# Kernel optimization log

Hardware: AMD Instinct MI355X
Metric: run time of the kernel (lower is better)

Reference implementation:

```python
import jax, jax.numpy as jnp
import numpy as np

N = 50000
E = 800000
C = 128   # embed_channels
H = 4     # num_heads
D = C // H
POS = 3


def setup_inputs() -> dict:
    key = jax.random.key(0)
    ks = jax.random.split(key, 8)
    feat = jax.random.normal(ks[0], (N, C), dtype=jnp.float32)
    coord = jax.random.normal(ks[1], (N, POS), dtype=jnp.float32)
    graph = jax.random.randint(ks[2], (2, E), 0, N, dtype=jnp.int32)
    qkv_w = jax.random.normal(ks[3], (3 * C, C), dtype=jnp.float32) * (1.0 / np.sqrt(C))
    qkv_b = jax.random.normal(ks[4], (3 * C,), dtype=jnp.float32) * 0.02
    rpe_w = jax.random.normal(ks[5], (C, POS), dtype=jnp.float32) * (1.0 / np.sqrt(POS))
    rpe_b = jax.random.normal(ks[6], (C,), dtype=jnp.float32) * 0.02
    return {"feat": feat, "coord": coord, "graph": graph,
            "qkv_w": qkv_w, "qkv_b": qkv_b, "rpe_w": rpe_w, "rpe_b": rpe_b}


def _segment_softmax(x, seg, n):
    # x: [E, H], seg: [E] -> softmax over edges sharing the same destination node
    seg_max = jax.ops.segment_max(x, seg, num_segments=n)          # [N, H]
    seg_max = jnp.where(jnp.isfinite(seg_max), seg_max, 0.0)
    ex = jnp.exp(x - seg_max[seg])                                 # [E, H]
    seg_sum = jax.ops.segment_sum(ex, seg, num_segments=n)         # [N, H]
    return ex / seg_sum[seg]


def reference(feat, coord, graph, qkv_w, qkv_b, rpe_w, rpe_b):
    n = feat.shape[0]
    # qkv projection: [N, 3C] -> [N, 3, H, D]
    qkv = (feat @ qkv_w.T + qkv_b).reshape(n, 3, H, D)
    query, key, value = qkv[:, 0], qkv[:, 1], qkv[:, 2]            # each [N, H, D]
    dst, src = graph[0], graph[1]                                  # [E]
    # relative position encoding per edge
    rel = coord[dst] - coord[src]                                  # [E, 3]
    rpe = (rel @ rpe_w.T + rpe_b).reshape(-1, H, D)                # [E, H, D]
    # per-edge attention logits
    attn = (key[src] * query[dst] + rpe).sum(-1)                   # [E, H]
    attn = _segment_softmax(attn, dst, n)                          # [E, H]
    # weighted scatter-sum of values
    msg = attn[..., None] * value[src]                             # [E, H, D]
    out = jax.ops.segment_sum(msg, dst, num_segments=n)            # [N, H, D]
    return out.reshape(n, H * D)
```

## Files before the change

kernel.cpp:

```cpp
#include <hip/hip_runtime.h>
#include <hip/hip_bf16.h>

#define NN 50000
#define NE 800000
#define PAD 64
#define CAB 196
#define NBK 391
#define CAPB 2560
#define GB_STRIDE 32

typedef _Float16 fp16x8 __attribute__((ext_vector_type(8)));
typedef _Float16 half2 __attribute__((ext_vector_type(2)));
typedef __attribute__((ext_vector_type(8))) unsigned short ushort8;
typedef __attribute__((ext_vector_type(4))) float f32x4;

static __device__ __forceinline__ unsigned short f2h(float x) {
    _Float16 h = (_Float16)x;
    return __builtin_bit_cast(unsigned short, h);
}
static __device__ __forceinline__ float dot2(half2 a, half2 b, float c) {
#if __has_builtin(__builtin_amdgcn_fdot2)
    return __builtin_amdgcn_fdot2(a, b, c, false);
#else
    return c + (float)a.x * (float)b.x + (float)a.y * (float)b.y;
#endif
}

__global__ __launch_bounds__(256) void qkv_gemm(
    const float* __restrict__ feat, const float* __restrict__ w,
    const float* __restrict__ bias, unsigned short* __restrict__ qbuf16,
    unsigned short* __restrict__ kvbuf,
    const float* __restrict__ coord, const float* __restrict__ rpe_w,
    const float* __restrict__ rpe_b, float* __restrict__ ca,
    float* __restrict__ cb,
    const int* __restrict__ graph, unsigned int* __restrict__ gbase,
    unsigned int* __restrict__ ebuf)
{
    const int t    = threadIdx.x;
    const int role = blockIdx.x & 3;
    const int bi   = blockIdx.x >> 2;

    __shared__ __align__(16) unsigned short Ah[128][40];
    __shared__ __align__(16) unsigned short Bh[128][40];

    if (role == 3) {
        unsigned int* hist  = (unsigned int*)&Ah[0][0];
        unsigned int* sbase = hist + 512;
        for (int u = t; u < NBK; u += 256) hist[u] = 0u;
        __syncthreads();

        int dsts[8], srcs[8];
        bool ok[8];
        const int e0 = bi * 2048;
#pragma unroll
        for (int u = 0; u < 8; ++u) {
            int e = e0 + u * 256 + t;
            ok[u] = (e < NE);
            if (ok[u]) { dsts[u] = graph[e]; srcs[u] = graph[NE + e]; }
        }
#pragma unroll
        for (int u = 0; u < 8; ++u)
            if (ok[u]) atomicAdd(&hist[dsts[u] >> 7], 1u);
        __syncthreads();
        for (int u = t; u < NBK; u += 256) {
            unsigned int c = hist[u];
            unsigned int s = c ? atomicAdd(&gbase[u * GB_STRIDE], c) : 0u;
            sbase[u] = s;
            hist[u]  = 0u;
        }
        __syncthreads();
#pragma unroll
        for (int u = 0; u < 8; ++u)
            if (ok[u]) {
                int b = dsts[u] >> 7;
                unsigned int pos = sbase[b] + atomicAdd(&hist[b], 1u);
                if (pos < CAPB)
                    ebuf[(size_t)b * CAPB + pos] =
                        ((unsigned int)(dsts[u] & 127) << 16) | (unsigned int)srcs[u];
            }

        if (bi < CAB) {
            __shared__ float s_rw[12];
            __shared__ float s_rb[4];
            if (t < 12) {
                int h = t / 3, p = t % 3;
                float s = 0.f;
                for (int d = 0; d < 32; ++d) s += rpe_w[(h * 32 + d) * 3 + p];
                s_rw[t] = s;
            } else if (t < 16) {
                int h = t - 12;
                float s = 0.f;
                for (int d = 0; d < 32; ++d) s += rpe_b[h * 32 + d];
                s_rb[h] = s;
            }
            __syncthreads();
            int n = bi * 256 + t;
            if (n < NN) {
                float c0 = coord[n * 3 + 0], c1 = coord[n * 3 + 1], c2 = coord[n * 3 + 2];
#pragma unroll
                for (int h = 0; h < 4; ++h) {
                    float a = c0 * s_rw[h * 3 + 0] + c1 * s_rw[h * 3 + 1] + c2 * s_rw[h * 3 + 2];
                    ca[n * 4 + h] = a;
                    cb[n * 4 + h] = a + s_rb[h];
                }
            }
        }
        return;
    }

    const int bm = bi * 128;
    const int bc = role * 128;

    const int wave = t >> 6;
    const int lane = t & 63;
    const int wr = wave & 1;
    const int wc = wave >> 1;
    const int qd = lane >> 4;
    const int l15 = lane & 15;

    f32x4 acc[4][4];
#pragma unroll
    for (int i = 0; i < 4; ++i)
#pragma unroll
        for (int j = 0; j < 4; ++j)
            acc[i][j] = (f32x4){0.f, 0.f, 0.f, 0.f};

    for (int ks = 0; ks < 4; ++ks) {
        const int k0 = ks * 32;
        if (ks) __syncthreads();
#pragma unroll
        for (int c = 0; c < 2; ++c) {
            int idx = c * 256 + t;
            int r  = idx >> 2;
            int c8 = (idx & 3) * 8;
            int ga = bm + r;
            ushort8 a8 = (ushort8){0,0,0,0,0,0,0,0};
            if (ga < NN) {
                const float* ap = feat + (size_t)ga * 128 + k0 + c8;
                float4 x = *(const float4*)ap;
                float4 y = *(const float4*)(ap + 4);
                a8 = (ushort8){f2h(x.x), f2h(x.y), f2h(x.z), f2h(x.w),
                               f2h(y.x), f2h(y.y), f2h(y.z), f2h(y.w)};
            }
            *(ushort8*)&Ah[r][c8] = a8;
            const float* bp = w + (size_t)(bc + r) * 128 + k0 + c8;
            float4 bx = *(const float4*)bp;
            float4 by = *(const float4*)(bp + 4);
            *(ushort8*)&Bh[r][c8] = (ushort8){f2h(bx.x), f2h(bx.y), f2h(bx.z), f2h(bx.w),
                                              f2h(by.x), f2h(by.y), f2h(by.z), f2h(by.w)};
        }
        __syncthreads();
        fp16x8 af[4];
#pragma unroll
        for (int i = 0; i < 4; ++i)
            af[i] = *(const fp16x8*)&Ah[wr * 64 + 16 * i + l15][qd * 8];
#pragma unroll
        for (int j = 0; j < 4; ++j) {
            fp16x8 bf = *(const fp16x8*)&Bh[wc * 64 + 16 * j + l15][qd * 8];
#pragma unroll
            for (int i = 0; i < 4; ++i)
                acc[i][j] = __builtin_amdgcn_mfma_f32_16x16x32_f16(af[i], bf, acc[i][j], 0, 0, 0);
        }
    }

    float bj[4];
#pragma unroll
    for (int j = 0; j < 4; ++j)
        bj[j] = bias[bc + wc * 64 + 16 * j + l15];

    unsigned short* Ct = &Ah[0][0];
    const int isQ = (role == 0);
    const int half = (role == 1) ? 0 : 128;
    const int relRowW = wr * 16 + qd * 4;

    for (int i = 0; i < 4; ++i) {
        __syncthreads();
#pragma unroll
        for (int j = 0; j < 4; ++j) {
            int col = wc * 64 + 16 * j + l15;
#pragma unroll
            for (int rg = 0; rg < 4; ++rg)
                Ct[(relRowW + rg) * 136 + col] = f2h(acc[i][j][rg] + bj[j]);
        }
        __syncthreads();
#pragma unroll
        for (int p = 0; p < 2; ++p) {
            int linear = p * 256 + t;
            int rr = linear >> 4;
            int cc = linear & 15;
            int absRow = bm + 16 * i + rr + ((rr >> 4) * 48);
            if (absRow < NN) {
                ushort8 val = *(const ushort8*)&Ct[rr * 136 + cc * 8];
                if (isQ) *(ushort8*)(qbuf16 + (size_t)absRow * 128 + cc * 8) = val;
                else     *(ushort8*)(kvbuf + (size_t)absRow * 256 + half + cc * 8) = val;
            }
        }
    }
}

__global__ __launch_bounds__(256) void bucket_to_csr(
    const unsigned int* __restrict__ gbase, const unsigned int* __restrict__ ebuf,
    int* __restrict__ cnt, unsigned short* __restrict__ sorted_src)
{
    __shared__ unsigned int ncnt[128];
    const int b = blockIdx.x;
    const int t = threadIdx.x;
    if (t < 128) ncnt[t] = 0u;
    __syncthreads();

    int total = (int)gbase[b * GB_STRIDE];
    if (total > CAPB) total = CAPB;
    const unsigned int* eb = ebuf + (size_t)b * CAPB;
    for (int i = t; i < total; i += 256) {
        unsigned int e = eb[i];
        int dl = (int)(e >> 16);
        unsigned int slot = atomicAdd(&ncnt[dl], 1u);
        if (slot < PAD)
            sorted_src[(((size_t)(b * 128 + dl)) << 6) + slot] =
                (unsigned short)(e & 0xFFFFu);
    }
    __syncthreads();
    if (t < 128) {
        int node = b * 128 + t;
        if (node < NN) {
            unsigned int c = ncnt[t];
            cnt[node] = (c > PAD) ? PAD : (int)c;
        }
    }
}

__global__ __launch_bounds__(256) void node_attn(
    const unsigned short* __restrict__ qbuf16, const unsigned short* __restrict__ kvbuf,
    const float* __restrict__ ca, const float* __restrict__ cb,
    const int* __restrict__ cnt, const unsigned short* __restrict__ sorted_src,
    float* __restrict__ out)
{
    const int t = threadIdx.x;
    const int n = blockIdx.x * 8 + (t >> 5);
    if (n >= NN) return;
    const int j = t & 31;
    const int h = j >> 3;
    const int j8 = j * 8;
    const int h4 = h * 4;

    const uint2 qv = *(const uint2*)((const char*)qbuf16 + (size_t)n * 256 + j8);
    const half2 qh01 = __builtin_bit_cast(half2, qv.x);
    const half2 qh23 = __builtin_bit_cast(half2, qv.y);
    const float cbh = cb[n * 4 + h];
    const int start = n << 6;
    int d = cnt[n];
    if (d > PAD) d = PAD;

    float4 acc = make_float4(0.f, 0.f, 0.f, 0.f);
    float den = 0.f;
    const char* kvp = (const char*)kvbuf;
    const char* cap = (const char*)ca;

    int i = 0;
    for (; i + 7 < d; i += 8) {
        ushort8 s8 = *(const ushort8*)(sorted_src + start + i);
        unsigned o[8];
#pragma unroll
        for (int u = 0; u < 8; ++u) o[u] = (unsigned)s8[u] << 9;
        uint2 kk[8], vv[8];
        float aa[8];
#pragma unroll
        for (int u = 0; u < 8; ++u) kk[u] = *(const uint2*)(kvp + o[u] + j8);
#pragma unroll
        for (int u = 0; u < 8; ++u) vv[u] = *(const uint2*)(kvp + o[u] + 256 + j8);
#pragma unroll
        for (int u = 0; u < 8; ++u) aa[u] = *(const float*)(cap + (o[u] >> 5) + h4);
        float p[8];
#pragma unroll
        for (int u = 0; u < 8; ++u)
            p[u] = dot2(qh01, __builtin_bit_cast(half2, kk[u].x),
                   dot2(qh23, __builtin_bit_cast(half2, kk[u].y), 0.f));
#pragma unroll
        for (int u = 0; u < 8; ++u) p[u] += __shfl_xor(p[u], 1);
#pragma unroll
        for (int u = 0; u < 8; ++u) p[u] += __shfl_xor(p[u], 2);
#pragma unroll
        for (int u = 0; u < 8; ++u) p[u] += __shfl_xor(p[u], 4);
        float e[8];
#pragma unroll
        for (int u = 0; u < 8; ++u) { e[u] = __expf(p[u] + cbh - aa[u]); den += e[u]; }
#pragma unroll
        for (int u = 0; u < 8; ++u) {
            half2 va = __builtin_bit_cast(half2, vv[u].x);
            half2 vb = __builtin_bit_cast(half2, vv[u].y);
            acc.x += e[u] * (float)va.x;
            acc.y += e[u] * (float)va.y;
            acc.z += e[u] * (float)vb.x;
            acc.w += e[u] * (float)vb.y;
        }
    }
    for (; i + 3 < d; i += 4) {
        ushort4 s4 = *(const ushort4*)(sorted_src + start + i);
        unsigned o0 = (unsigned)s4.x << 9;
        unsigned o1 = (unsigned)s4.y << 9;
        unsigned o2 = (unsigned)s4.z << 9;
        unsigned o3 = (unsigned)s4.w << 9;
        uint2 k0 = *(const uint2*)(kvp + o0 + j8);
        uint2 k1 = *(const uint2*)(kvp + o1 + j8);
        uint2 k2 = *(const uint2*)(kvp + o2 + j8);
        uint2 k3 = *(const uint2*)(kvp + o3 + j8);
        uint2 v0 = *(const uint2*)(kvp + o0 + 256 + j8);
        uint2 v1 = *(const uint2*)(kvp + o1 + 256 + j8);
        uint2 v2 = *(const uint2*)(kvp + o2 + 256 + j8);
        uint2 v3 = *(const uint2*)(kvp + o3 + 256 + j8);
        float a0 = *(const float*)(cap + (o0 >> 5) + h4);
        float a1 = *(const float*)(cap + (o1 >> 5) + h4);
        float a2 = *(const float*)(cap + (o2 >> 5) + h4);
        float a3 = *(const float*)(cap + (o3 >> 5) + h4);

        float p0 = dot2(qh01, __builtin_bit_cast(half2, k0.x),
                   dot2(qh23, __builtin_bit_cast(half2, k0.y), 0.f));
        float p1 = dot2(qh01, __builtin_bit_cast(half2, k1.x),
                   dot2(qh23, __builtin_bit_cast(half2, k1.y), 0.f));
        float p2 = dot2(qh01, __builtin_bit_cast(half2, k2.x),
                   dot2(qh23, __builtin_bit_cast(half2, k2.y), 0.f));
        float p3 = dot2(qh01, __builtin_bit_cast(half2, k3.x),
                   dot2(qh23, __builtin_bit_cast(half2, k3.y), 0.f));
        p0 += __shfl_xor(p0, 1); p1 += __shfl_xor(p1, 1);
        p2 += __shfl_xor(p2, 1); p3 += __shfl_xor(p3, 1);
        p0 += __shfl_xor(p0, 2); p1 += __shfl_xor(p1, 2);
        p2 += __shfl_xor(p2, 2); p3 += __shfl_xor(p3, 2);
        p0 += __shfl_xor(p0, 4); p1 += __shfl_xor(p1, 4);
        p2 += __shfl_xor(p2, 4); p3 += __shfl_xor(p3, 4);

        float e0 = __expf(p0 + cbh - a0);
        float e1 = __expf(p1 + cbh - a1);
        float e2 = __expf(p2 + cbh - a2);
        float e3 = __expf(p3 + cbh - a3);
        den += (e0 + e1) + (e2 + e3);
        half2 v0a = __builtin_bit_cast(half2, v0.x), v0b = __builtin_bit_cast(half2, v0.y);
        half2 v1a = __builtin_bit_cast(half2, v1.x), v1b = __builtin_bit_cast(half2, v1.y);
        half2 v2a = __builtin_bit_cast(half2, v2.x), v2b = __builtin_bit_cast(half2, v2.y);
        half2 v3a = __builtin_bit_cast(half2, v3.x), v3b = __builtin_bit_cast(half2, v3.y);
        acc.x += e0 * (float)v0a.x + e1 * (float)v1a.x + e2 * (float)v2a.x + e3 * (float)v3a.x;
        acc.y += e0 * (float)v0a.y + e1 * (float)v1a.y + e2 * (float)v2a.y + e3 * (float)v3a.y;
        acc.z += e0 * (float)v0b.x + e1 * (float)v1b.x + e2 * (float)v2b.x + e3 * (float)v3b.x;
        acc.w += e0 * (float)v0b.y + e1 * (float)v1b.y + e2 * (float)v2b.y + e3 * (float)v3b.y;
    }
    for (; i < d; ++i) {
        unsigned o0 = (unsigned)sorted_src[start + i] << 9;
        uint2 k0 = *(const uint2*)(kvp + o0 + j8);
        uint2 v0 = *(const uint2*)(kvp + o0 + 256 + j8);
        float a0 = *(const float*)(cap + (o0 >> 5) + h4);
        float p0 = dot2(qh01, __builtin_bit_cast(half2, k0.x),
                   dot2(qh23, __builtin_bit_cast(half2, k0.y), 0.f));
        p0 += __shfl_xor(p0, 1);
        p0 += __shfl_xor(p0, 2);
        p0 += __shfl_xor(p0, 4);
        float e = __expf(p0 + cbh - a0);
        den += e;
        half2 va = __builtin_bit_cast(half2, v0.x);
        half2 vb = __builtin_bit_cast(half2, v0.y);
        acc.x += e * (float)va.x;
        acc.y += e * (float)va.y;
        acc.z += e * (float)vb.x;
        acc.w += e * (float)vb.y;
    }

    float inv = (den > 0.f) ? 1.0f / den : 0.f;
    float4 o = make_float4(acc.x * inv, acc.y * inv, acc.z * inv, acc.w * inv);
    ((float4*)(out + (size_t)n * 128))[j] = o;
}

extern "C" void kernel_launch(void* const* d_in, const int* in_sizes, int n_in,
                              void* d_out, int out_size, void* d_ws, size_t ws_size,
                              hipStream_t stream) {
    const float* feat  = (const float*)d_in[0];
    const float* coord = (const float*)d_in[1];
    const int*   graph = (const int*)d_in[2];
    const float* qkv_w = (const float*)d_in[3];
    const float* qkv_b = (const float*)d_in[4];
    const float* rpe_w = (const float*)d_in[5];
    const float* rpe_b = (const float*)d_in[6];
    float* out = (float*)d_out;

    unsigned short* qbuf16 = (unsigned short*)d_ws;
    unsigned short* kvbuf  = qbuf16 + (size_t)NN * 128;
    int*            cnt    = (int*)(kvbuf + (size_t)NN * 256);
    unsigned short* sorted_src = (unsigned short*)(cnt + NN);
    float* ca = (float*)(sorted_src + (size_t)NN * PAD);
    float* cb = ca + (size_t)NN * 4;
    unsigned int* gbase = (unsigned int*)(cb + (size_t)NN * 4);
    unsigned int* ebuf  = gbase + (size_t)NBK * GB_STRIDE;

    hipMemsetAsync(gbase, 0, (size_t)NBK * GB_STRIDE * sizeof(unsigned int), stream);

    qkv_gemm <<<dim3(391 * 4), 256, 0, stream>>>(feat, qkv_w, qkv_b, qbuf16, kvbuf,
                                                 coord, rpe_w, rpe_b, ca, cb,
                                                 graph, gbase, ebuf);
    bucket_to_csr<<<dim3(NBK), 256, 0, stream>>>(gbase, ebuf, cnt, sorted_src);
    node_attn<<<dim3((NN + 7) / 8), 256, 0, stream>>>(qbuf16, kvbuf, ca, cb,
                                                      cnt, sorted_src, out);
}
```

Measured before the change: 185.7 us.

## Split attention into score and output kernels with head-major K/V layout

K and V are now stored head-major, as separate [H][N][32] fp16 arrays instead of one interleaved [N][256] buffer. The fused node attention kernel is split into two. The first computes per-edge exp scores per head and stores them with the inverse denominators in a workspace buffer. The second gathers V per head and accumulates the output. The head-major layout gives each pass a smaller gather footprint that fits better in cache, at the cost of an extra launch, a round trip of the score buffer through memory, and a second read of the CSR indices.

Result: slower. 225.5 us (+21.4%).

```diff
diff --git a/kernel.cpp b/kernel.cpp
--- a/kernel.cpp
+++ b/kernel.cpp
@@ -8,6 +8,8 @@
 #define NBK 391
 #define CAPB 2560
 #define GB_STRIDE 32
+#define NCHUNK 1563
+#define NPAIR 782
 
 typedef _Float16 fp16x8 __attribute__((ext_vector_type(8)));
 typedef _Float16 half2 __attribute__((ext_vector_type(2)));
@@ -25,11 +27,14 @@
     return c + (float)a.x * (float)b.x + (float)a.y * (float)b.y;
 #endif
 }
+static __device__ __forceinline__ half2 h2(unsigned u) {
+    return __builtin_bit_cast(half2, u);
+}
 
 __global__ __launch_bounds__(256) void qkv_gemm(
     const float* __restrict__ feat, const float* __restrict__ w,
     const float* __restrict__ bias, unsigned short* __restrict__ qbuf16,
-    unsigned short* __restrict__ kvbuf,
+    unsigned short* __restrict__ kh, unsigned short* __restrict__ vh,
     const float* __restrict__ coord, const float* __restrict__ rpe_w,
     const float* __restrict__ rpe_b, float* __restrict__ ca,
     float* __restrict__ cb,
@@ -170,7 +175,7 @@
 
     unsigned short* Ct = &Ah[0][0];
     const int isQ = (role == 0);
-    const int half = (role == 1) ? 0 : 128;
+    unsigned short* kv_dst = (role == 1) ? kh : vh;
     const int relRowW = wr * 16 + qd * 4;
 
     for (int i = 0; i < 4; ++i) {
@@ -191,8 +196,12 @@
             int absRow = bm + 16 * i + rr + ((rr >> 4) * 48);
             if (absRow < NN) {
                 ushort8 val = *(const ushort8*)&Ct[rr * 136 + cc * 8];
-                if (isQ) *(ushort8*)(qbuf16 + (size_t)absRow * 128 + cc * 8) = val;
-                else     *(ushort8*)(kvbuf + (size_t)absRow * 256 + half + cc * 8) = val;
+                if (isQ) {
+                    *(ushort8*)(qbuf16 + (size_t)absRow * 128 + cc * 8) = val;
+                } else {
+                    size_t off = (size_t)(cc >> 2) * NN * 32 + (size_t)absRow * 32 + (cc & 3) * 8;
+                    *(ushort8*)(kv_dst + off) = val;
+                }
             }
         }
     }
@@ -229,142 +238,127 @@
     }
 }
 
-__global__ __launch_bounds__(256) void node_attn(
-    const unsigned short* __restrict__ qbuf16, const unsigned short* __restrict__ kvbuf,
+__global__ __launch_bounds__(256) void attn_score(
+    const unsigned short* __restrict__ qbuf16, const unsigned short* __restrict__ kh,
     const float* __restrict__ ca, const float* __restrict__ cb,
     const int* __restrict__ cnt, const unsigned short* __restrict__ sorted_src,
-    float* __restrict__ out)
+    float* __restrict__ ebufE, float* __restrict__ invden)
 {
     const int t = threadIdx.x;
-    const int n = blockIdx.x * 8 + (t >> 5);
+    const int x = blockIdx.x & 7;
+    const int h = x >> 1;
+    const int chunk = (blockIdx.x >> 3) * 2 + (x & 1);
+    const int n = chunk * 32 + (t >> 3);
     if (n >= NN) return;
-    const int j = t & 31;
-    const int h = j >> 3;
-    const int j8 = j * 8;
-    const int h4 = h * 4;
-
-    const uint2 qv = *(const uint2*)((const char*)qbuf16 + (size_t)n * 256 + j8);
-    const half2 qh01 = __builtin_bit_cast(half2, qv.x);
-    const half2 qh23 = __builtin_bit_cast(half2, qv.y);
+    const int l  = t & 7;
+    const int l4 = l * 4;
+
+    const uint2 qv = *(const uint2*)(qbuf16 + (size_t)n * 128 + h * 32 + l4);
+    const half2 q01 = h2(qv.x), q23 = h2(qv.y);
     const float cbh = cb[n * 4 + h];
-    const int start = n << 6;
+    const unsigned short* sl  = sorted_src + ((size_t)n << 6);
+    const unsigned short* khp = kh + (size_t)h * NN * 32;
+    float* erow = ebufE + ((size_t)h * NN + n) * 64;
     int d = cnt[n];
-    if (d > PAD) d = PAD;
-
-    float4 acc = make_float4(0.f, 0.f, 0.f, 0.f);
+
     float den = 0.f;
-    const char* kvp = (const char*)kvbuf;
-    const char* cap = (const char*)ca;
-
     int i = 0;
-    for (; i + 7 < d; i += 8) {
-        ushort8 s8 = *(const ushort8*)(sorted_src + start + i);
-        unsigned o[8];
-#pragma unroll
-        for (int u = 0; u < 8; ++u) o[u] = (unsigned)s8[u] << 9;
-        uint2 kk[8], vv[8];
-        float aa[8];
-#pragma unroll
-        for (int u = 0; u < 8; ++u) kk[u] = *(const uint2*)(kvp + o[u] + j8);
-#pragma unroll
-        for (int u = 0; u < 8; ++u) vv[u] = *(const uint2*)(kvp + o[u] + 256 + j8);
-#pragma unroll
-        for (int u = 0; u < 8; ++u) aa[u] = *(const float*)(cap + (o[u] >> 5) + h4);
-        float p[8];
-#pragma unroll
-        for (int u = 0; u < 8; ++u)
-            p[u] = dot2(qh01, __builtin_bit_cast(half2, kk[u].x),
-                   dot2(qh23, __builtin_bit_cast(half2, kk[u].y), 0.f));
-#pragma unroll
-        for (int u = 0; u < 8; ++u) p[u] += __shfl_xor(p[u], 1);
-#pragma unroll
-        for (int u = 0; u < 8; ++u) p[u] += __shfl_xor(p[u], 2);
-#pragma unroll
-        for (int u = 0; u < 8; ++u) p[u] += __shfl_xor(p[u], 4);
-        float e[8];
-#pragma unroll
-        for (int u = 0; u < 8; ++u) { e[u] = __expf(p[u] + cbh - aa[u]); den += e[u]; }
-#pragma unroll
-        for (int u = 0; u < 8; ++u) {
-            half2 va = __builtin_bit_cast(half2, vv[u].x);
-            half2 vb = __builtin_bit_cast(half2, vv[u].y);
-            acc.x += e[u] * (float)va.x;
-            acc.y += e[u] * (float)va.y;
-            acc.z += e[u] * (float)vb.x;
-            acc.w += e[u] * (float)vb.y;
-        }
-    }
     for (; i + 3 < d; i += 4) {
-        ushort4 s4 = *(const ushort4*)(sorted_src + start + i);
-        unsigned o0 = (unsigned)s4.x << 9;
-        unsigned o1 = (unsigned)s4.y << 9;
-        unsigned o2 = (unsigned)s4.z << 9;
-        unsigned o3 = (unsigned)s4.w << 9;
-        uint2 k0 = *(const uint2*)(kvp + o0 + j8);
-        uint2 k1 = *(const uint2*)(kvp + o1 + j8);
-        uint2 k2 = *(const uint2*)(kvp + o2 + j8);
-        uint2 k3 = *(const uint2*)(kvp + o3 + j8);
-        uint2 v0 = *(const uint2*)(kvp + o0 + 256 + j8);
-        uint2 v1 = *(const uint2*)(kvp + o1 + 256 + j8);
-        uint2 v2 = *(const uint2*)(kvp + o2 + 256 + j8);
-        uint2 v3 = *(const uint2*)(kvp + o3 + 256 + j8);
-        float a0 = *(const float*)(cap + (o0 >> 5) + h4);
-        float a1 = *(const float*)(cap + (o1 >> 5) + h4);
-        float a2 = *(const float*)(cap + (o2 >> 5) + h4);
-        float a3 = *(const float*)(cap + (o3 >> 5) + h4);
-
-        float p0 = dot2(qh01, __builtin_bit_cast(half2, k0.x),
-                   dot2(qh23, __builtin_bit_cast(half2, k0.y), 0.f));
-        float p1 = dot2(qh01, __builtin_bit_cast(half2, k1.x),
-                   dot2(qh23, __builtin_bit_cast(half2, k1.y), 0.f));
-        float p2 = dot2(qh01, __builtin_bit_cast(half2, k2.x),
-                   dot2(qh23, __builtin_bit_cast(half2, k2.y), 0.f));
-        float p3 = dot2(qh01, __builtin_bit_cast(half2, k3.x),
-                   dot2(qh23, __builtin_bit_cast(half2, k3.y), 0.f));
-        p0 += __shfl_xor(p0, 1); p1 += __shfl_xor(p1, 1);
-        p2 += __shfl_xor(p2, 1); p3 += __shfl_xor(p3, 1);
-        p0 += __shfl_xor(p0, 2); p1 += __shfl_xor(p1, 2);
-        p2 += __shfl_xor(p2, 2); p3 += __shfl_xor(p3, 2);
-        p0 += __shfl_xor(p0, 4); p1 += __shfl_xor(p1, 4);
-        p2 += __shfl_xor(p2, 4); p3 += __shfl_xor(p3, 4);
-
-        float e0 = __expf(p0 + cbh - a0);
-        float e1 = __expf(p1 + cbh - a1);
-        float e2 = __expf(p2 + cbh - a2);
-        float e3 = __expf(p3 + cbh - a3);
-        den += (e0 + e1) + (e2 + e3);
-        half2 v0a = __builtin_bit_cast(half2, v0.x), v0b = __builtin_bit_cast(half2, v0.y);
-        half2 v1a = __builtin_bit_cast(half2, v1.x), v1b = __builtin_bit_cast(half2, v1.y);
-        half2 v2a = __builtin_bit_cast(half2, v2.x), v2b = __builtin_bit_cast(half2, v2.y);
-        half2 v3a = __builtin_bit_cast(half2, v3.x), v3b = __builtin_bit_cast(half2, v3.y);
-        acc.x += e0 * (float)v0a.x + e1 * (float)v1a.x + e2 * (float)v2a.x + e3 * (float)v3a.x;
-        acc.y += e0 * (float)v0a.y + e1 * (float)v1a.y + e2 * (float)v2a.y + e3 * (float)v3a.y;
-        acc.z += e0 * (float)v0b.x + e1 * (float)v1b.x + e2 * (float)v2b.x + e3 * (float)v3b.x;
-        acc.w += e0 * (float)v0b.y + e1 * (float)v1b.y + e2 * (float)v2b.y + e3 * (float)v3b.y;
+        ushort4 s4 = *(const ushort4*)(sl + i);
+        uint2 kk[4];
+        float aa[4];
+        kk[0] = *(const uint2*)(khp + (size_t)s4.x * 32 + l4);
+        kk[1] = *(const uint2*)(khp + (size_t)s4.y * 32 + l4);
+        kk[2] = *(const uint2*)(khp + (size_t)s4.z * 32 + l4);
+        kk[3] = *(const uint2*)(khp + (size_t)s4.w * 32 + l4);
+        aa[0] = ca[(int)s4.x * 4 + h];
+        aa[1] = ca[(int)s4.y * 4 + h];
+        aa[2] = ca[(int)s4.z * 4 + h];
+        aa[3] = ca[(int)s4.w * 4 + h];
+        float p[4];
+#pragma unroll
+        for (int u = 0; u < 4; ++u)
+            p[u] = dot2(q01, h2(kk[u].x), dot2(q23, h2(kk[u].y), 0.f));
+#pragma unroll
+        for (int u = 0; u < 4; ++u) {
+            p[u] += __shfl_xor(p[u], 1);
+            p[u] += __shfl_xor(p[u], 2);
+            p[u] += __shfl_xor(p[u], 4);
+        }
+        float e[4];
+#pragma unroll
+        for (int u = 0; u < 4; ++u) { e[u] = __expf(p[u] + cbh - aa[u]); den += e[u]; }
+        if (l == 0) *(float4*)(erow + i) = make_float4(e[0], e[1], e[2], e[3]);
     }
     for (; i < d; ++i) {
-        unsigned o0 = (unsigned)sorted_src[start + i] << 9;
-        uint2 k0 = *(const uint2*)(kvp + o0 + j8);
-        uint2 v0 = *(const uint2*)(kvp + o0 + 256 + j8);
-        float a0 = *(const float*)(cap + (o0 >> 5) + h4);
-        float p0 = dot2(qh01, __builtin_bit_cast(half2, k0.x),
-                   dot2(qh23, __builtin_bit_cast(half2, k0.y), 0.f));
+        unsigned s = sl[i];
+        uint2 k0 = *(const uint2*)(khp + (size_t)s * 32 + l4);
+        float a0 = ca[(int)s * 4 + h];
+        float p0 = dot2(q01, h2(k0.x), dot2(q23, h2(k0.y), 0.f));
         p0 += __shfl_xor(p0, 1);
         p0 += __shfl_xor(p0, 2);
         p0 += __shfl_xor(p0, 4);
         float e = __expf(p0 + cbh - a0);
         den += e;
-        half2 va = __builtin_bit_cast(half2, v0.x);
-        half2 vb = __builtin_bit_cast(half2, v0.y);
-        acc.x += e * (float)va.x;
-        acc.y += e * (float)va.y;
-        acc.z += e * (float)vb.x;
-        acc.w += e * (float)vb.y;
-    }
-
-    float inv = (den > 0.f) ? 1.0f / den : 0.f;
+        if (l == 0) erow[i] = e;
+    }
+    if (l == 0) invden[n * 4 + h] = (den > 0.f) ? 1.0f / den : 0.f;
+}
+
+__global__ __launch_bounds__(256) void attn_out(
+    const unsigned short* __restrict__ vh,
+    const int* __restrict__ cnt, const unsigned short* __restrict__ sorted_src,
+    const float* __restrict__ ebufE, const float* __restrict__ invden,
+    float* __restrict__ out)
+{
+    const int t = threadIdx.x;
+    const int x = blockIdx.x & 7;
+    const int h = x >> 1;
+    const int chunk = (blockIdx.x >> 3) * 2 + (x & 1);
+    const int n = chunk * 32 + (t >> 3);
+    if (n >= NN) return;
+    const int l  = t & 7;
+    const int l4 = l * 4;
+
+    const unsigned short* sl  = sorted_src + ((size_t)n << 6);
+    const unsigned short* vhp = vh + (size_t)h * NN * 32;
+    const float* erow = ebufE + ((size_t)h * NN + n) * 64;
+    int d = cnt[n];
+
+    float4 acc = make_float4(0.f, 0.f, 0.f, 0.f);
+    int i = 0;
+    for (; i + 3 < d; i += 4) {
+        ushort4 s4 = *(const ushort4*)(sl + i);
+        float4 ef = *(const float4*)(erow + i);
+        uint2 vv[4];
+        vv[0] = *(const uint2*)(vhp + (size_t)s4.x * 32 + l4);
+        vv[1] = *(const uint2*)(vhp + (size_t)s4.y * 32 + l4);
+        vv[2] = *(const uint2*)(vhp + (size_t)s4.z * 32 + l4);
+        vv[3] = *(const uint2*)(vhp + (size_t)s4.w * 32 + l4);
+        float ee[4] = {ef.x, ef.y, ef.z, ef.w};
+#pragma unroll
+        for (int u = 0; u < 4; ++u) {
+            half2 a = h2(vv[u].x), b = h2(vv[u].y);
+            acc.x += ee[u] * (float)a.x;
+            acc.y += ee[u] * (float)a.y;
+            acc.z += ee[u] * (float)b.x;
+            acc.w += ee[u] * (float)b.y;
+        }
+    }
+    for (; i < d; ++i) {
+        unsigned s = sl[i];
+        float e = erow[i];
+        uint2 v0 = *(const uint2*)(vhp + (size_t)s * 32 + l4);
+        half2 a = h2(v0.x), b = h2(v0.y);
+        acc.x += e * (float)a.x;
+        acc.y += e * (float)a.y;
+        acc.z += e * (float)b.x;
+        acc.w += e * (float)b.y;
+    }
+
+    const float inv = invden[n * 4 + h];
     float4 o = make_float4(acc.x * inv, acc.y * inv, acc.z * inv, acc.w * inv);
-    ((float4*)(out + (size_t)n * 128))[j] = o;
+    *(float4*)(out + (size_t)n * 128 + h * 32 + l4) = o;
 }
 
 extern "C" void kernel_launch(void* const* d_in, const int* in_sizes, int n_in,
@@ -380,20 +374,25 @@
     float* out = (float*)d_out;
 
     unsigned short* qbuf16 = (unsigned short*)d_ws;
-    unsigned short* kvbuf  = qbuf16 + (size_t)NN * 128;
-    int*            cnt    = (int*)(kvbuf + (size_t)NN * 256);
+    unsigned short* kh     = qbuf16 + (size_t)NN * 128;
+    unsigned short* vh     = kh + (size_t)NN * 128;
+    int*            cnt    = (int*)(vh + (size_t)NN * 128);
     unsigned short* sorted_src = (unsigned short*)(cnt + NN);
     float* ca = (float*)(sorted_src + (size_t)NN * PAD);
     float* cb = ca + (size_t)NN * 4;
     unsigned int* gbase = (unsigned int*)(cb + (size_t)NN * 4);
     unsigned int* ebuf  = gbase + (size_t)NBK * GB_STRIDE;
+    float* ebufE  = (float*)(ebuf + (size_t)NBK * CAPB);
+    float* invden = ebufE + (size_t)4 * NN * 64;
 
     hipMemsetAsync(gbase, 0, (size_t)NBK * GB_STRIDE * sizeof(unsigned int), stream);
 
-    qkv_gemm <<<dim3(391 * 4), 256, 0, stream>>>(feat, qkv_w, qkv_b, qbuf16, kvbuf,
+    qkv_gemm <<<dim3(391 * 4), 256, 0, stream>>>(feat, qkv_w, qkv_b, qbuf16, kh, vh,
                                                  coord, rpe_w, rpe_b, ca, cb,
                                                  graph, gbase, ebuf);
     bucket_to_csr<<<dim3(NBK), 256, 0, stream>>>(gbase, ebuf, cnt, sorted_src);
-    node_attn<<<dim3((NN + 7) / 8), 256, 0, stream>>>(qbuf16, kvbuf, ca, cb,
-                                                      cnt, sorted_src, out);
-}
+    attn_score<<<dim3(NPAIR * 8), 256, 0, stream>>>(qbuf16, kh, ca, cb,
+                                                    cnt, sorted_src, ebufE, invden);
+    attn_out  <<<dim3(NPAIR * 8), 256, 0, stream>>>(vh, cnt, sorted_src,
+                                                    ebufE, invden, out);
+}
```

## Fuse bucket-to-CSR sort into node attention kernel using LDS slot lists

Applied to the files above, without the earlier changes.

Removes the separate bucket_to_csr kernel and the sorted_src/cnt global buffers. Each attention block now rescans its bucket's edge list, keeps only the edges for its 32-node quarter, builds per-node source lists in shared memory, and then runs the same gather-softmax-accumulate loop over those nodes. This saves a kernel launch and a global write/read round trip of the CSR arrays. The cost is that every bucket's edge list is read four times, once per quarter-block, and each block does more serial work. The GEMM block index mapping is also remapped so blocks of the same role are grouped in runs of eight, changing the scheduling order.

After: 182.1 us. No clear change (-1.9%).

```diff
diff --git a/kernel.cpp b/kernel.cpp
--- a/kernel.cpp
+++ b/kernel.cpp
@@ -24,6 +24,9 @@
 #else
     return c + (float)a.x * (float)b.x + (float)a.y * (float)b.y;
 #endif
+}
+static __device__ __forceinline__ half2 h2(unsigned u) {
+    return __builtin_bit_cast(half2, u);
 }
 
 __global__ __launch_bounds__(256) void qkv_gemm(
@@ -36,9 +39,18 @@
     const int* __restrict__ graph, unsigned int* __restrict__ gbase,
     unsigned int* __restrict__ ebuf)
 {
-    const int t    = threadIdx.x;
-    const int role = blockIdx.x & 3;
-    const int bi   = blockIdx.x >> 2;
+    const int t  = threadIdx.x;
+    const int bx = blockIdx.x;
+    int bi, role;
+    if (bx < 1536) {
+        int rem = bx & 31;
+        role = rem >> 3;
+        bi   = (bx >> 5) * 8 + (rem & 7);
+    } else {
+        int idx = bx - 1536;
+        role = idx / 7;
+        bi   = 384 + idx - role * 7;
+    }
 
     __shared__ __align__(16) unsigned short Ah[128][40];
     __shared__ __align__(16) unsigned short Bh[128][40];
@@ -144,10 +156,10 @@
             }
             *(ushort8*)&Ah[r][c8] = a8;
             const float* bp = w + (size_t)(bc + r) * 128 + k0 + c8;
-            float4 bx = *(const float4*)bp;
-            float4 by = *(const float4*)(bp + 4);
-            *(ushort8*)&Bh[r][c8] = (ushort8){f2h(bx.x), f2h(bx.y), f2h(bx.z), f2h(bx.w),
-                                              f2h(by.x), f2h(by.y), f2h(by.z), f2h(by.w)};
+            float4 bx2 = *(const float4*)bp;
+            float4 by2 = *(const float4*)(bp + 4);
+            *(ushort8*)&Bh[r][c8] = (ushort8){f2h(bx2.x), f2h(bx2.y), f2h(bx2.z), f2h(bx2.w),
+                                              f2h(by2.x), f2h(by2.y), f2h(by2.z), f2h(by2.w)};
         }
         __syncthreads();
         fp16x8 af[4];
@@ -198,14 +210,20 @@
     }
 }
 
-__global__ __launch_bounds__(256) void bucket_to_csr(
+__global__ __launch_bounds__(256) void attn_fused(
+    const unsigned short* __restrict__ qbuf16, const unsigned short* __restrict__ kvbuf,
+    const float* __restrict__ ca, const float* __restrict__ cb,
     const unsigned int* __restrict__ gbase, const unsigned int* __restrict__ ebuf,
-    int* __restrict__ cnt, unsigned short* __restrict__ sorted_src)
+    float* __restrict__ out)
 {
-    __shared__ unsigned int ncnt[128];
-    const int b = blockIdx.x;
-    const int t = threadIdx.x;
-    if (t < 128) ncnt[t] = 0u;
+    __shared__ __align__(16) unsigned short slots[32][64];
+    __shared__ unsigned int ncnt[32];
+
+    const int t    = threadIdx.x;
+    const int b    = blockIdx.x >> 2;
+    const int quad = blockIdx.x & 3;
+
+    if (t < 32) ncnt[t] = 0u;
     __syncthreads();
 
     int total = (int)gbase[b * GB_STRIDE];
@@ -214,157 +232,142 @@
     for (int i = t; i < total; i += 256) {
         unsigned int e = eb[i];
         int dl = (int)(e >> 16);
-        unsigned int slot = atomicAdd(&ncnt[dl], 1u);
-        if (slot < PAD)
-            sorted_src[(((size_t)(b * 128 + dl)) << 6) + slot] =
-                (unsigned short)(e & 0xFFFFu);
+        if ((dl >> 5) == quad) {
+            int ldl = dl & 31;
+            unsigned int slot = atomicAdd(&ncnt[ldl], 1u);
+            if (slot < PAD) slots[ldl][slot] = (unsigned short)(e & 0xFFFFu);
+        }
     }
     __syncthreads();
-    if (t < 128) {
-        int node = b * 128 + t;
-        if (node < NN) {
-            unsigned int c = ncnt[t];
-            cnt[node] = (c > PAD) ? PAD : (int)c;
-        }
-    }
-}
-
-__global__ __launch_bounds__(256) void node_attn(
-    const unsigned short* __restrict__ qbuf16, const unsigned short* __restrict__ kvbuf,
-    const float* __restrict__ ca, const float* __restrict__ cb,
-    const int* __restrict__ cnt, const unsigned short* __restrict__ sorted_src,
-    float* __restrict__ out)
-{
-    const int t = threadIdx.x;
-    const int n = blockIdx.x * 8 + (t >> 5);
-    if (n >= NN) return;
-    const int j = t & 31;
-    const int h = j >> 3;
+
+    const int j  = t & 31;
+    const int h  = j >> 3;
     const int j8 = j * 8;
     const int h4 = h * 4;
-
-    const uint2 qv = *(const uint2*)((const char*)qbuf16 + (size_t)n * 256 + j8);
-    const half2 qh01 = __builtin_bit_cast(half2, qv.x);
-    const half2 qh23 = __builtin_bit_cast(half2, qv.y);
-    const float cbh = cb[n * 4 + h];
-    const int start = n << 6;
-    int d = cnt[n];
-    if (d > PAD) d = PAD;
-
-    float4 acc = make_float4(0.f, 0.f, 0.f, 0.f);
-    float den = 0.f;
+    const int ln = t >> 5;
     const char* kvp = (const char*)kvbuf;
     const char* cap = (const char*)ca;
 
-    int i = 0;
-    for (; i + 7 < d; i += 8) {
-        ushort8 s8 = *(const ushort8*)(sorted_src + start + i);
-        unsigned o[8];
-#pragma unroll
-        for (int u = 0; u < 8; ++u) o[u] = (unsigned)s8[u] << 9;
-        uint2 kk[8], vv[8];
-        float aa[8];
-#pragma unroll
-        for (int u = 0; u < 8; ++u) kk[u] = *(const uint2*)(kvp + o[u] + j8);
-#pragma unroll
-        for (int u = 0; u < 8; ++u) vv[u] = *(const uint2*)(kvp + o[u] + 256 + j8);
-#pragma unroll
-        for (int u = 0; u < 8; ++u) aa[u] = *(const float*)(cap + (o[u] >> 5) + h4);
-        float p[8];
-#pragma unroll
-        for (int u = 0; u < 8; ++u)
-            p[u] = dot2(qh01, __builtin_bit_cast(half2, kk[u].x),
-                   dot2(qh23, __builtin_bit_cast(half2, kk[u].y), 0.f));
-#pragma unroll
-        for (int u = 0; u < 8; ++u) p[u] += __shfl_xor(p[u], 1);
-#pragma unroll
-        for (int u = 0; u < 8; ++u) p[u] += __shfl_xor(p[u], 2);
-#pragma unroll
-        for (int u = 0; u < 8; ++u) p[u] += __shfl_xor(p[u], 4);
-        float e[8];
-#pragma unroll
-        for (int u = 0; u < 8; ++u) { e[u] = __expf(p[u] + cbh - aa[u]); den += e[u]; }
-#pragma unroll
-        for (int u = 0; u < 8; ++u) {
-            half2 va = __builtin_bit_cast(half2, vv[u].x);
-            half2 vb = __builtin_bit_cast(half2, vv[u].y);
-            acc.x += e[u] * (float)va.x;
-            acc.y += e[u] * (float)va.y;
-            acc.z += e[u] * (float)vb.x;
-            acc.w += e[u] * (float)vb.y;
-        }
-    }
-    for (; i + 3 < d; i += 4) {
-        ushort4 s4 = *(const ushort4*)(sorted_src + start + i);
-        unsigned o0 = (unsigned)s4.x << 9;
-        unsigned o1 = (unsigned)s4.y << 9;
-        unsigned o2 = (unsigned)s4.z << 9;
-        unsigned o3 = (unsigned)s4.w << 9;
-        uint2 k0 = *(const uint2*)(kvp + o0 + j8);
-        uint2 k1 = *(const uint2*)(kvp + o1 + j8);
-        uint2 k2 = *(const uint2*)(kvp + o2 + j8);
-        uint2 k3 = *(const uint2*)(kvp + o3 + j8);
-        uint2 v0 = *(const uint2*)(kvp + o0 + 256 + j8);
-        uint2 v1 = *(const uint2*)(kvp + o1 + 256 + j8);
-        uint2 v2 = *(const uint2*)(kvp + o2 + 256 + j8);
-        uint2 v3 = *(const uint2*)(kvp + o3 + 256 + j8);
-        float a0 = *(const float*)(cap + (o0 >> 5) + h4);
-        float a1 = *(const float*)(cap + (o1 >> 5) + h4);
-        float a2 = *(const float*)(cap + (o2 >> 5) + h4);
-        float a3 = *(const float*)(cap + (o3 >> 5) + h4);
-
-        float p0 = dot2(qh01, __builtin_bit_cast(half2, k0.x),
-                   dot2(qh23, __builtin_bit_cast(half2, k0.y), 0.f));
-        float p1 = dot2(qh01, __builtin_bit_cast(half2, k1.x),
-                   dot2(qh23, __builtin_bit_cast(half2, k1.y), 0.f));
-        float p2 = dot2(qh01, __builtin_bit_cast(half2, k2.x),
-                   dot2(qh23, __builtin_bit_cast(half2, k2.y), 0.f));
-        float p3 = dot2(qh01, __builtin_bit_cast(half2, k3.x),
-                   dot2(qh23, __builtin_bit_cast(half2, k3.y), 0.f));
-        p0 += __shfl_xor(p0, 1); p1 += __shfl_xor(p1, 1);
-        p2 += __shfl_xor(p2, 1); p3 += __shfl_xor(p3, 1);
-        p0 += __shfl_xor(p0, 2); p1 += __shfl_xor(p1, 2);
-        p2 += __shfl_xor(p2, 2); p3 += __shfl_xor(p3, 2);
-        p0 += __shfl_xor(p0, 4); p1 += __shfl_xor(p1, 4);
-        p2 += __shfl_xor(p2, 4); p3 += __shfl_xor(p3, 4);
-
-        float e0 = __expf(p0 + cbh - a0);
-        float e1 = __expf(p1 + cbh - a1);
-        float e2 = __expf(p2 + cbh - a2);
-        float e3 = __expf(p3 + cbh - a3);
-        den += (e0 + e1) + (e2 + e3);
-        half2 v0a = __builtin_bit_cast(half2, v0.x), v0b = __builtin_bit_cast(half2, v0.y);
-        half2 v1a = __builtin_bit_cast(half2, v1.x), v1b = __builtin_bit_cast(half2, v1.y);
-        half2 v2a = __builtin_bit_cast(half2, v2.x), v2b = __builtin_bit_cast(half2, v2.y);
-        half2 v3a = __builtin_bit_cast(half2, v3.x), v3b = __builtin_bit_cast(half2, v3.y);
-        acc.x += e0 * (float)v0a.x + e1 * (float)v1a.x + e2 * (float)v2a.x + e3 * (float)v3a.x;
-        acc.y += e0 * (float)v0a.y + e1 * (float)v1a.y + e2 * (float)v2a.y + e3 * (float)v3a.y;
-        acc.z += e0 * (float)v0b.x + e1 * (float)v1b.x + e2 * (float)v2b.x + e3 * (float)v3b.x;
-        acc.w += e0 * (float)v0b.y + e1 * (float)v1b.y + e2 * (float)v2b.y + e3 * (float)v3b.y;
-    }
-    for (; i < d; ++i) {
-        unsigned o0 = (unsigned)sorted_src[start + i] << 9;
-        uint2 k0 = *(const uint2*)(kvp + o0 + j8);
-        uint2 v0 = *(const uint2*)(kvp + o0 + 256 + j8);
-        float a0 = *(const float*)(cap + (o0 >> 5) + h4);
-        float p0 = dot2(qh01, __builtin_bit_cast(half2, k0.x),
-                   dot2(qh23, __builtin_bit_cast(half2, k0.y), 0.f));
-        p0 += __shfl_xor(p0, 1);
-        p0 += __shfl_xor(p0, 2);
-        p0 += __shfl_xor(p0, 4);
-        float e = __expf(p0 + cbh - a0);
-        den += e;
-        half2 va = __builtin_bit_cast(half2, v0.x);
-        half2 vb = __builtin_bit_cast(half2, v0.y);
-        acc.x += e * (float)va.x;
-        acc.y += e * (float)va.y;
-        acc.z += e * (float)vb.x;
-        acc.w += e * (float)vb.y;
-    }
-
-    float inv = (den > 0.f) ? 1.0f / den : 0.f;
-    float4 o = make_float4(acc.x * inv, acc.y * inv, acc.z * inv, acc.w * inv);
-    ((float4*)(out + (size_t)n * 128))[j] = o;
+    for (int g = 0; g < 4; ++g) {
+        const int ldl = g * 8 + ln;
+        const int n = b * 128 + quad * 32 + ldl;
+        if (n >= NN) continue;
+        int d = (int)ncnt[ldl];
+        if (d > PAD) d = PAD;
+        const unsigned short* sl = &slots[ldl][0];
+
+        const uint2 qv = *(const uint2*)((const char*)qbuf16 + (size_t)n * 256 + j8);
+        const half2 qh01 = h2(qv.x);
+        const half2 qh23 = h2(qv.y);
+        const float cbh = cb[n * 4 + h];
+
+        float4 acc = make_float4(0.f, 0.f, 0.f, 0.f);
+        float den = 0.f;
+
+        int i = 0;
+        for (; i + 7 < d; i += 8) {
+            ushort8 s8 = *(const ushort8*)(sl + i);
+            unsigned o[8];
+#pragma unroll
+            for (int u = 0; u < 8; ++u) o[u] = (unsigned)s8[u] << 9;
+            uint2 kk[8], vv[8];
+            float aa[8];
+#pragma unroll
+            for (int u = 0; u < 8; ++u) kk[u] = *(const uint2*)(kvp + o[u] + j8);
+#pragma unroll
+            for (int u = 0; u < 8; ++u) vv[u] = *(const uint2*)(kvp + o[u] + 256 + j8);
+#pragma unroll
+            for (int u = 0; u < 8; ++u) aa[u] = *(const float*)(cap + (o[u] >> 5) + h4);
+            float p[8];
+#pragma unroll
+            for (int u = 0; u < 8; ++u)
+                p[u] = dot2(qh01, h2(kk[u].x), dot2(qh23, h2(kk[u].y), 0.f));
+#pragma unroll
+            for (int u = 0; u < 8; ++u) p[u] += __shfl_xor(p[u], 1);
+#pragma unroll
+            for (int u = 0; u < 8; ++u) p[u] += __shfl_xor(p[u], 2);
+#pragma unroll
+            for (int u = 0; u < 8; ++u) p[u] += __shfl_xor(p[u], 4);
+            float e[8];
+#pragma unroll
+            for (int u = 0; u < 8; ++u) { e[u] = __expf(p[u] + cbh - aa[u]); den += e[u]; }
+#pragma unroll
+            for (int u = 0; u < 8; ++u) {
+                half2 va = h2(vv[u].x);
+                half2 vb = h2(vv[u].y);
+                acc.x += e[u] * (float)va.x;
+                acc.y += e[u] * (float)va.y;
+                acc.z += e[u] * (float)vb.x;
+                acc.w += e[u] * (float)vb.y;
+            }
+        }
+        for (; i + 3 < d; i += 4) {
+            ushort4 s4 = *(const ushort4*)(sl + i);
+            unsigned o0 = (unsigned)s4.x << 9;
+            unsigned o1 = (unsigned)s4.y << 9;
+            unsigned o2 = (unsigned)s4.z << 9;
+            unsigned o3 = (unsigned)s4.w << 9;
+            uint2 k0 = *(const uint2*)(kvp + o0 + j8);
+            uint2 k1 = *(const uint2*)(kvp + o1 + j8);
+            uint2 k2 = *(const uint2*)(kvp + o2 + j8);
+            uint2 k3 = *(const uint2*)(kvp + o3 + j8);
+            uint2 v0 = *(const uint2*)(kvp + o0 + 256 + j8);
+            uint2 v1 = *(const uint2*)(kvp + o1 + 256 + j8);
+            uint2 v2 = *(const uint2*)(kvp + o2 + 256 + j8);
+            uint2 v3 = *(const uint2*)(kvp + o3 + 256 + j8);
+            float a0 = *(const float*)(cap + (o0 >> 5) + h4);
+            float a1 = *(const float*)(cap + (o1 >> 5) + h4);
+            float a2 = *(const float*)(cap + (o2 >> 5) + h4);
+            float a3 = *(const float*)(cap + (o3 >> 5) + h4);
+
+            float p0 = dot2(qh01, h2(k0.x), dot2(qh23, h2(k0.y), 0.f));
+            float p1 = dot2(qh01, h2(k1.x), dot2(qh23, h2(k1.y), 0.f));
+            float p2 = dot2(qh01, h2(k2.x), dot2(qh23, h2(k2.y), 0.f));
+            float p3 = dot2(qh01, h2(k3.x), dot2(qh23, h2(k3.y), 0.f));
+            p0 += __shfl_xor(p0, 1); p1 += __shfl_xor(p1, 1);
+            p2 += __shfl_xor(p2, 1); p3 += __shfl_xor(p3, 1);
+            p0 += __shfl_xor(p0, 2); p1 += __shfl_xor(p1, 2);
+            p2 += __shfl_xor(p2, 2); p3 += __shfl_xor(p3, 2);
+            p0 += __shfl_xor(p0, 4); p1 += __shfl_xor(p1, 4);
+            p2 += __shfl_xor(p2, 4); p3 += __shfl_xor(p3, 4);
+
+            float e0 = __expf(p0 + cbh - a0);
+            float e1 = __expf(p1 + cbh - a1);
+            float e2 = __expf(p2 + cbh - a2);
+            float e3 = __expf(p3 + cbh - a3);
+            den += (e0 + e1) + (e2 + e3);
+            half2 v0a = h2(v0.x), v0b = h2(v0.y);
+            half2 v1a = h2(v1.x), v1b = h2(v1.y);
+            half2 v2a = h2(v2.x), v2b = h2(v2.y);
+            half2 v3a = h2(v3.x), v3b = h2(v3.y);
+            acc.x += e0 * (float)v0a.x + e1 * (float)v1a.x + e2 * (float)v2a.x + e3 * (float)v3a.x;
+            acc.y += e0 * (float)v0a.y + e1 * (float)v1a.y + e2 * (float)v2a.y + e3 * (float)v3a.y;
+            acc.z += e0 * (float)v0b.x + e1 * (float)v1b.x + e2 * (float)v2b.x + e3 * (float)v3b.x;
+            acc.w += e0 * (float)v0b.y + e1 * (float)v1b.y + e2 * (float)v2b.y + e3 * (float)v3b.y;
+        }
+        for (; i < d; ++i) {
+            unsigned o0 = (unsigned)sl[i] << 9;
+            uint2 k0 = *(const uint2*)(kvp + o0 + j8);
+            uint2 v0 = *(const uint2*)(kvp + o0 + 256 + j8);
+            float a0 = *(const float*)(cap + (o0 >> 5) + h4);
+            float p0 = dot2(qh01, h2(k0.x), dot2(qh23, h2(k0.y), 0.f));
+            p0 += __shfl_xor(p0, 1);
+            p0 += __shfl_xor(p0, 2);
+            p0 += __shfl_xor(p0, 4);
+            float e = __expf(p0 + cbh - a0);
+            den += e;
+            half2 va = h2(v0.x);
+            half2 vb = h2(v0.y);
+            acc.x += e * (float)va.x;
+            acc.y += e * (float)va.y;
+            acc.z += e * (float)vb.x;
+            acc.w += e * (float)vb.y;
+        }
+
+        float inv = (den > 0.f) ? 1.0f / den : 0.f;
+        float4 o = make_float4(acc.x * inv, acc.y * inv, acc.z * inv, acc.w * inv);
+        ((float4*)(out + (size_t)n * 128))[j] = o;
+    }
 }
 
 extern "C" void kernel_launch(void* const* d_in, const int* in_sizes, int n_in,
@@ -381,19 +384,16 @@
 
     unsigned short* qbuf16 = (unsigned short*)d_ws;
     unsigned short* kvbuf  = qbuf16 + (size_t)NN * 128;
-    int*            cnt    = (int*)(kvbuf + (size_t)NN * 256);
-    unsigned short* sorted_src = (unsigned short*)(cnt + NN);
-    float* ca = (float*)(sorted_src + (size_t)NN * PAD);
+    float* ca = (float*)(kvbuf + (size_t)NN * 256);
     float* cb = ca + (size_t)NN * 4;
     unsigned int* gbase = (unsigned int*)(cb + (size_t)NN * 4);
     unsigned int* ebuf  = gbase + (size_t)NBK * GB_STRIDE;
 
     hipMemsetAsync(gbase, 0, (size_t)NBK * GB_STRIDE * sizeof(unsigned int), stream);
 
-    qkv_gemm <<<dim3(391 * 4), 256, 0, stream>>>(feat, qkv_w, qkv_b, qbuf16, kvbuf,
-                                                 coord, rpe_w, rpe_b, ca, cb,
-                                                 graph, gbase, ebuf);
-    bucket_to_csr<<<dim3(NBK), 256, 0, stream>>>(gbase, ebuf, cnt, sorted_src);
-    node_attn<<<dim3((NN + 7) / 8), 256, 0, stream>>>(qbuf16, kvbuf, ca, cb,
-                                                      cnt, sorted_src, out);
-}
+    qkv_gemm  <<<dim3(391 * 4), 256, 0, stream>>>(feat, qkv_w, qkv_b, qbuf16, kvbuf,
+                                                  coord, rpe_w, rpe_b, ca, cb,
+                                                  graph, gbase, ebuf);
+    attn_fused<<<dim3(NBK * 4), 256, 0, stream>>>(qbuf16, kvbuf, ca, cb,
+                                                  gbase, ebuf, out);
+}
```
